# Performance work log

Measured on AMD Instinct MI355X. Metric: run time of the kernel, lower is better.

## Reference

```python
import jax, jax.numpy as jnp
import numpy as np

B = 256   # batch (bs)
N = 6890  # SMPL vertices
J = 24    # joints (root + 23)
NB = 10   # betas
P = 100   # points per foot plane
PARENTS = np.array([-1,0,0,0,1,2,3,4,5,6,7,8,9,9,9,12,13,14,16,17,18,19,20,21], dtype=np.int64)


def setup_inputs() -> dict:
    key = jax.random.key(0)
    ks = jax.random.split(key, 20)
    v_template = jax.random.normal(ks[0], (N, 3), jnp.float32) * 0.3
    shapedirs = jax.random.normal(ks[1], (N, 3, NB), jnp.float32) * 0.01
    Jr = jax.random.uniform(ks[2], (J, N), jnp.float32)
    J_regressor = Jr / Jr.sum(axis=1, keepdims=True)
    lw = jax.random.uniform(ks[3], (N, J), jnp.float32)
    lbs_weights = lw / lw.sum(axis=1, keepdims=True)
    betas = jnp.concatenate([jnp.ones((1, 1), jnp.float32),
                             jax.random.normal(ks[4], (1, NB), jnp.float32) * 0.5], axis=1)
    return dict(
        v_template=v_template, shapedirs=shapedirs, J_regressor=J_regressor,
        lbs_weights=lbs_weights, betas=betas,
        body_pose_wo_foot=jax.random.normal(ks[5], (B, 57), jnp.float32) * 0.2,
        r_back_foot_pose=jax.random.normal(ks[6], (B, 3), jnp.float32) * 0.2,
        r_front_foot_pose=jax.random.normal(ks[7], (B,), jnp.float32) * 0.2,
        l_back_foot_pose=jax.random.normal(ks[8], (B, 3), jnp.float32) * 0.2,
        l_front_foot_pose=jax.random.normal(ks[9], (B,), jnp.float32) * 0.2,
        transl=jax.random.normal(ks[10], (B, 3), jnp.float32) * 0.1,
        global_orient=jax.random.normal(ks[11], (B, 3), jnp.float32) * 0.2,
        init_plane_back_l=jax.random.normal(ks[12], (B, P, 3), jnp.float32) * 0.1,
        init_plane_front_l=jax.random.normal(ks[13], (B, P, 3), jnp.float32) * 0.1,
        init_plane_back_r=jax.random.normal(ks[14], (B, P, 3), jnp.float32) * 0.1,
        init_plane_front_r=jax.random.normal(ks[15], (B, P, 3), jnp.float32) * 0.1,
        parents=jnp.asarray(PARENTS),
        foot_back_l_ids=jax.random.randint(ks[16], (P,), 0, N),
        foot_back_r_ids=jax.random.randint(ks[17], (P,), 0, N),
        foot_front_l_ids=jax.random.randint(ks[18], (P,), 0, N),
        foot_front_r_ids=jax.random.randint(ks[19], (P,), 0, N),
    )


def _rodrigues(rot_vecs):
    # rot_vecs: [M,3] axis-angle -> [M,3,3] rotation matrices (matches SMPL batch_rodrigues)
    angle = jnp.linalg.norm(rot_vecs + 1e-8, axis=1, keepdims=True)  # [M,1]
    rot_dir = rot_vecs / angle
    cos = jnp.cos(angle)[..., None]  # [M,1,1]
    sin = jnp.sin(angle)[..., None]
    rx, ry, rz = rot_dir[:, 0], rot_dir[:, 1], rot_dir[:, 2]
    zeros = jnp.zeros_like(rx)
    K = jnp.stack([zeros, -rz, ry, rz, zeros, -rx, -ry, rx, zeros], axis=1).reshape(-1, 3, 3)
    I = jnp.eye(3, dtype=rot_vecs.dtype)
    return I + sin * K + (1.0 - cos) * jnp.matmul(K, K)


def _forward(v_template, shapedirs, J_regressor, lbs_weights, betas,
             body_pose_wo_foot, r_back_foot_pose, r_front_foot_pose,
             l_back_foot_pose, l_front_foot_pose, transl, global_orient,
             init_plane_back_l, init_plane_front_l, init_plane_back_r, init_plane_front_r,
             ids):
    Bn = body_pose_wo_foot.shape[0]
    dt = v_template.dtype
    # --- update_shape ---
    blend = jnp.einsum('bl,mkl->bmk', betas[:, 1:], shapedirs)            # [1,N,3]
    v_shaped = (v_template[None] + blend) * betas[:, 0][:, None, None]    # [1,N,3]
    J_shaped = jnp.einsum('bik,ji->bjk', v_shaped, J_regressor)           # [1,J,3]
    # --- assemble full pose (foot-joint splicing) ---
    z2 = jnp.zeros((Bn, 2), dt)
    body_pose = jnp.concatenate([
        body_pose_wo_foot[:, :18],              # joints 1..6
        l_back_foot_pose,                       # joint 7
        r_back_foot_pose,                       # joint 8
        body_pose_wo_foot[:, 18:21],            # joint 9
        l_front_foot_pose[:, None], z2,         # joint 10 (x only)
        r_front_foot_pose[:, None], z2,         # joint 11 (x only)
        body_pose_wo_foot[:, 21:]], axis=1)     # joints 12..23
    full_pose = jnp.concatenate([global_orient, body_pose], axis=1)      # [B,72]
    rot = _rodrigues(full_pose.reshape(-1, 3)).reshape(Bn, J, 3, 3)
    # --- batch_rigid_transform ---
    joints = jnp.broadcast_to(J_shaped, (Bn, J, 3))
    rel = jnp.concatenate([joints[:, :1], joints[:, 1:] - joints[:, PARENTS[1:]]], axis=1)
    top = jnp.concatenate([rot, rel[..., None]], axis=-1)                 # [B,J,3,4]
    bottom = jnp.broadcast_to(jnp.array([0., 0., 0., 1.], dt), (Bn, J, 1, 4))
    T_loc = jnp.concatenate([top, bottom], axis=2)                        # [B,J,4,4]
    chain = [T_loc[:, 0]]
    for i in range(1, J):  # fixed 24-joint kinematic chain
        chain.append(chain[int(PARENTS[i])] @ T_loc[:, i])
    transforms = jnp.stack(chain, axis=1)                                 # [B,J,4,4]
    J_transformed = transforms[..., :3, 3]
    init_bone = jnp.einsum('bjmn,bjn->bjm', transforms[..., :3, :3], joints)
    A = transforms.at[..., :3, 3].add(-init_bone)                         # relative transforms
    # --- LBS skinning ---
    T = jnp.einsum('vj,bjmn->bvmn', lbs_weights, A)                       # [B,N,4,4]
    verts = jnp.einsum('bvmn,vn->bvm', T[:, :, :3, :3], v_shaped[0]) + T[:, :, :3, 3] + transl[:, None]
    # --- foot planes ---
    def _plane(idx, init):
        Tp = T[:, idx]                                                    # [B,P,4,4]
        return jnp.einsum('bpmn,bpn->bpm', Tp[:, :, :3, :3], init) + Tp[:, :, :3, 3]
    bl, fl, br, fr = ids
    v_plane = jnp.concatenate([
        _plane(bl, init_plane_back_l), _plane(fl, init_plane_front_l),
        _plane(br, init_plane_back_r), _plane(fr, init_plane_front_r)], axis=1) + transl[:, None]
    return verts, J_transformed, v_plane


def reference(v_template, shapedirs, J_regressor, lbs_weights, betas,
              body_pose_wo_foot, r_back_foot_pose, r_front_foot_pose,
              l_back_foot_pose, l_front_foot_pose, transl, global_orient,
              init_plane_back_l, init_plane_front_l, init_plane_back_r, init_plane_front_r,
              parents, foot_back_l_ids, foot_back_r_ids, foot_front_l_ids, foot_front_r_ids):
    ids = (foot_back_l_ids, foot_front_l_ids, foot_back_r_ids, foot_front_r_ids)
    return _forward(v_template, shapedirs, J_regressor, lbs_weights, betas,
                    body_pose_wo_foot, r_back_foot_pose, r_front_foot_pose,
                    l_back_foot_pose, l_front_foot_pose, transl, global_orient,
                    init_plane_back_l, init_plane_front_l, init_plane_back_r, init_plane_front_r,
                    ids)
```

## Files before the change

kernel.cpp:

```cpp
#include <hip/hip_runtime.h>
#include <stdint.h>

#define NV 6890
#define NJ 24
#define NB_ 256
#define NP 100
#define MP 6912

typedef unsigned short u16;
typedef unsigned int u32;
typedef __attribute__((ext_vector_type(8))) short bf16x8;
typedef __attribute__((ext_vector_type(4))) float f32x4;

__device__ __forceinline__ u16 f2bf(float f) {
    u32 u = __float_as_uint(f);
    u += 0x7FFFu + ((u >> 16) & 1u);
    return (u16)(u >> 16);
}

__constant__ int c_par[24] = {-1,0,0,0,1,2,3,4,5,6,7,8,9,9,9,12,13,14,16,17,18,19,20,21};

#define O_VS 0
#define O_JS 20672
#define O_A  20800
#define O_WT 189056
#define O_AT 852608

#define OUT_JT   5291520
#define OUT_PLN  5309952

__global__ __launch_bounds__(256) void k_shape(const float* __restrict__ vt,
                                               const float* __restrict__ sd,
                                               const float* __restrict__ jreg,
                                               const float* __restrict__ betas,
                                               float* __restrict__ ws) {
    int bx = blockIdx.x;
    float b0 = betas[0];
    if (bx < 81) {
        int idx = bx * 256 + threadIdx.x;
        if (idx < NV * 3) {
            float acc = vt[idx];
            const float* row = sd + (size_t)idx * 10;
#pragma unroll
            for (int l = 0; l < 10; ++l) acc += betas[1 + l] * row[l];
            ws[O_VS + idx] = acc * b0;
        }
        return;
    }
    int j = bx - 81;
    int tid = threadIdx.x;
    float be[10];
#pragma unroll
    for (int l = 0; l < 10; ++l) be[l] = betas[1 + l];
    float s0 = 0.f, s1 = 0.f, s2 = 0.f;
    for (int i = tid; i < NV; i += 256) {
        float w = jreg[(size_t)j * NV + i];
        const float* sr = sd + (size_t)i * 30;
        const float* vr = vt + (size_t)i * 3;
        float c0 = vr[0], c1 = vr[1], c2 = vr[2];
#pragma unroll
        for (int l = 0; l < 10; ++l) {
            c0 += be[l] * sr[l];
            c1 += be[l] * sr[10 + l];
            c2 += be[l] * sr[20 + l];
        }
        s0 += w * (c0 * b0);
        s1 += w * (c1 * b0);
        s2 += w * (c2 * b0);
    }
    __shared__ float r0[256], r1[256], r2[256];
    r0[tid] = s0; r1[tid] = s1; r2[tid] = s2;
    __syncthreads();
    for (int off = 128; off > 0; off >>= 1) {
        if (tid < off) { r0[tid] += r0[tid + off]; r1[tid] += r1[tid + off]; r2[tid] += r2[tid + off]; }
        __syncthreads();
    }
    if (tid == 0) {
        ws[O_JS + j * 3 + 0] = r0[0];
        ws[O_JS + j * 3 + 1] = r1[0];
        ws[O_JS + j * 3 + 2] = r2[0];
    }
}

__global__ __launch_bounds__(256) void k_prep(const float* __restrict__ lw,
                                              const float* __restrict__ bpwf,
                                              const float* __restrict__ rback,
                                              const float* __restrict__ rfront,
                                              const float* __restrict__ lback,
                                              const float* __restrict__ lfront,
                                              const float* __restrict__ gor,
                                              float* __restrict__ ws,
                                              u16* __restrict__ wsu,
                                              float* __restrict__ out) {
    int bx = blockIdx.x;
    if (bx < 2592) {
        int idx = bx * 256 + threadIdx.x;
        int v = idx / 96, k = idx - 96 * v;
        u16 o = 0;
        if (v < NV) {
            int j = k >> 2, n = k & 3;
            float w = lw[(size_t)v * 24 + j];
            float h = (n < 3) ? ws[O_VS + v * 3 + n] : 1.0f;
            o = f2bf(w * h);
        }
        wsu[O_WT + idx] = o;
        return;
    }
    int b = bx - 2592;
    int j = threadIdx.x;
    const float* js = ws + O_JS;
    __shared__ float sT[24][12];
    __shared__ float sJ[24][3];
    if (j < 24) {
        float px, py, pz;
        if (j == 0)      { px = gor[b*3];   py = gor[b*3+1];   pz = gor[b*3+2]; }
        else if (j <= 6) { int o = b*57 + 3*(j-1); px = bpwf[o]; py = bpwf[o+1]; pz = bpwf[o+2]; }
        else if (j == 7) { px = lback[b*3]; py = lback[b*3+1]; pz = lback[b*3+2]; }
        else if (j == 8) { px = rback[b*3]; py = rback[b*3+1]; pz = rback[b*3+2]; }
        else if (j == 9) { int o = b*57 + 18;     px = bpwf[o]; py = bpwf[o+1]; pz = bpwf[o+2]; }
        else if (j == 10){ px = lfront[b];  py = 0.f; pz = 0.f; }
        else if (j == 11){ px = rfront[b];  py = 0.f; pz = 0.f; }
        else             { int o = b*57 + 21 + 3*(j-12); px = bpwf[o]; py = bpwf[o+1]; pz = bpwf[o+2]; }
        float ax = px + 1e-8f, ay = py + 1e-8f, az = pz + 1e-8f;
        float ang = sqrtf(ax*ax + ay*ay + az*az);
        float inv = 1.0f / ang;
        float dx = px * inv, dy = py * inv, dz = pz * inv;
        float c = cosf(ang), s = sinf(ang), t = 1.0f - c;
        sJ[j][0] = js[j*3]; sJ[j][1] = js[j*3+1]; sJ[j][2] = js[j*3+2];
        int p = c_par[j];
        float rx = sJ[j][0], ry = sJ[j][1], rz = sJ[j][2];
        if (p >= 0) { rx -= js[p*3]; ry -= js[p*3+1]; rz -= js[p*3+2]; }
        sT[j][0] = 1.f - t*(dy*dy + dz*dz);
        sT[j][1] = -s*dz + t*dx*dy;
        sT[j][2] =  s*dy + t*dx*dz;
        sT[j][3] = rx;
        sT[j][4] =  s*dz + t*dx*dy;
        sT[j][5] = 1.f - t*(dx*dx + dz*dz);
        sT[j][6] = -s*dx + t*dy*dz;
        sT[j][7] = ry;
        sT[j][8] = -s*dy + t*dx*dz;
        sT[j][9] =  s*dx + t*dy*dz;
        sT[j][10]= 1.f - t*(dx*dx + dy*dy);
        sT[j][11]= rz;
    }
    __syncthreads();
    if (j < 24) {
        int path[12]; int d = 0; int cur = j;
        while (cur >= 0) { path[d++] = cur; cur = c_par[cur]; }
        float g[12];
        int r = path[d - 1];
#pragma unroll
        for (int m = 0; m < 12; ++m) g[m] = sT[r][m];
        for (int i = d - 2; i >= 0; --i) {
            int n = path[i];
            float h[12];
#pragma unroll
            for (int row = 0; row < 3; ++row) {
                float a0 = g[row*4+0], a1 = g[row*4+1], a2 = g[row*4+2], a3 = g[row*4+3];
                h[row*4+0] = a0*sT[n][0] + a1*sT[n][4] + a2*sT[n][8];
                h[row*4+1] = a0*sT[n][1] + a1*sT[n][5] + a2*sT[n][9];
                h[row*4+2] = a0*sT[n][2] + a1*sT[n][6] + a2*sT[n][10];
                h[row*4+3] = a0*sT[n][3] + a1*sT[n][7] + a2*sT[n][11] + a3;
            }
#pragma unroll
            for (int m = 0; m < 12; ++m) g[m] = h[m];
        }
        size_t jo = (size_t)OUT_JT + ((size_t)b * 24 + j) * 3;
        out[jo+0] = g[3]; out[jo+1] = g[7]; out[jo+2] = g[11];
        float jx = sJ[j][0], jy = sJ[j][1], jz = sJ[j][2];
        float Av[12];
        Av[0]=g[0]; Av[1]=g[1]; Av[2]=g[2];   Av[3] = g[3]  - (g[0]*jx + g[1]*jy + g[2]*jz);
        Av[4]=g[4]; Av[5]=g[5]; Av[6]=g[6];   Av[7] = g[7]  - (g[4]*jx + g[5]*jy + g[6]*jz);
        Av[8]=g[8]; Av[9]=g[9]; Av[10]=g[10]; Av[11]= g[11] - (g[8]*jx + g[9]*jy + g[10]*jz);
        float* Ab = ws + O_A + ((size_t)b * 24 + j) * 12;
#pragma unroll
        for (int m = 0; m < 12; ++m) Ab[m] = Av[m];
        u16* at = wsu + O_AT;
#pragma unroll
        for (int m = 0; m < 3; ++m)
#pragma unroll
            for (int n = 0; n < 4; ++n)
                at[(size_t)(b*3 + m) * 96 + j*4 + n] = f2bf(Av[m*4 + n]);
    }
}

__global__ __launch_bounds__(256) void k_main(const u16* __restrict__ wsu,
                                              const float* __restrict__ ws,
                                              const float* __restrict__ lw,
                                              const float* __restrict__ transl,
                                              const int* __restrict__ ids_bl,
                                              const int* __restrict__ ids_fl,
                                              const int* __restrict__ ids_br,
                                              const int* __restrict__ ids_fr,
                                              const float* __restrict__ ip_bl,
                                              const float* __restrict__ ip_fl,
                                              const float* __restrict__ ip_br,
                                              const float* __restrict__ ip_fr,
                                              float* __restrict__ out) {
    if (blockIdx.y < 12) {
        __shared__ float ltile[64][66];
        const u16* wt = wsu + O_WT;
        const u16* at = wsu + O_AT;
        int lane = threadIdx.x & 63;
        int wave = threadIdx.x >> 6;
        int row_in = lane & 15, quad = lane >> 4;
        int v0 = blockIdx.x * 64 + wave * 16;
        int c0 = blockIdx.y * 64;

        f32x4 acc0 = {0.f,0.f,0.f,0.f}, acc1 = acc0, acc2 = acc0, acc3 = acc0;
#pragma unroll
        for (int kc = 0; kc < 96; kc += 32) {
            bf16x8 a  = *(const bf16x8*)(wt + (size_t)(v0 + row_in) * 96 + kc + quad * 8);
            bf16x8 b0 = *(const bf16x8*)(at + (size_t)(c0 +  0 + row_in) * 96 + kc + quad * 8);
            bf16x8 b1 = *(const bf16x8*)(at + (size_t)(c0 + 16 + row_in) * 96 + kc + quad * 8);
            bf16x8 b2 = *(const bf16x8*)(at + (size_t)(c0 + 32 + row_in) * 96 + kc + quad * 8);
            bf16x8 b3 = *(const bf16x8*)(at + (size_t)(c0 + 48 + row_in) * 96 + kc + quad * 8);
            acc0 = __builtin_amdgcn_mfma_f32_16x16x32_bf16(a, b0, acc0, 0, 0, 0);
            acc1 = __builtin_amdgcn_mfma_f32_16x16x32_bf16(a, b1, acc1, 0, 0, 0);
            acc2 = __builtin_amdgcn_mfma_f32_16x16x32_bf16(a, b2, acc2, 0, 0, 0);
            acc3 = __builtin_amdgcn_mfma_f32_16x16x32_bf16(a, b3, acc3, 0, 0, 0);
        }
        int vbase = wave * 16 + quad * 4;
#pragma unroll
        for (int s = 0; s < 4; ++s) {
            f32x4 acc = (s == 0) ? acc0 : (s == 1) ? acc1 : (s == 2) ? acc2 : acc3;
#pragma unroll
            for (int r = 0; r < 4; ++r)
                ltile[vbase + r][s * 16 + row_in] = acc[r];
        }
        __syncthreads();
        int vblk = blockIdx.x * 64;
        int bstart = c0 / 3;
        int bend = (c0 + 63) / 3;
        int tid = threadIdx.x;
        for (int b = bstart; b <= bend; ++b) {
            if (tid < 192) {
                int vl = tid / 3, m = tid - 3 * (tid / 3);
                int cl = b * 3 + m - c0;
                int v = vblk + vl;
                if (cl >= 0 && cl < 64 && v < NV)
                    out[((size_t)b * NV + v) * 3 + m] = ltile[vl][cl] + transl[b * 3 + m];
            }
            if (tid >= 192 && tid < 192 + 64) {
            }
        }
        return;
    }
    for (int idx = blockIdx.x * 256 + threadIdx.x; idx < NB_ * 400; idx += 108 * 256) {
        int b = idx / 400;
        int rr = idx - 400 * b;
        int plane = rr / 100;
        int p = rr - 100 * plane;
        const int* ids   = (plane == 0) ? ids_bl : (plane == 1) ? ids_fl : (plane == 2) ? ids_br : ids_fr;
        const float* ip  = (plane == 0) ? ip_bl  : (plane == 1) ? ip_fl  : (plane == 2) ? ip_br  : ip_fr;
        int vid = ids[p];
        const float* Ab = ws + O_A + (size_t)b * 288;
        const float* w = lw + (size_t)vid * 24;
        float T[12];
#pragma unroll
        for (int m = 0; m < 12; ++m) T[m] = 0.f;
#pragma unroll
        for (int j = 0; j < NJ; ++j) {
            float wj = w[j];
#pragma unroll
            for (int m = 0; m < 12; ++m) T[m] += wj * Ab[j * 12 + m];
        }
        size_t io = ((size_t)b * NP + p) * 3;
        float vx = ip[io+0], vy = ip[io+1], vz = ip[io+2];
        float ox = T[0]*vx + T[1]*vy + T[2]*vz  + T[3]  + transl[b*3+0];
        float oy = T[4]*vx + T[5]*vy + T[6]*vz  + T[7]  + transl[b*3+1];
        float oz = T[8]*vx + T[9]*vy + T[10]*vz + T[11] + transl[b*3+2];
        size_t o = (size_t)OUT_PLN + (size_t)idx * 3;
        out[o+0] = ox; out[o+1] = oy; out[o+2] = oz;
    }
}

extern "C" void kernel_launch(void* const* d_in, const int* in_sizes, int n_in,
                              void* d_out, int out_size, void* d_ws, size_t ws_size,
                              hipStream_t stream) {
    const float* vt     = (const float*)d_in[0];
    const float* sd     = (const float*)d_in[1];
    const float* jreg   = (const float*)d_in[2];
    const float* lw     = (const float*)d_in[3];
    const float* betas  = (const float*)d_in[4];
    const float* bpwf   = (const float*)d_in[5];
    const float* rback  = (const float*)d_in[6];
    const float* rfront = (const float*)d_in[7];
    const float* lback  = (const float*)d_in[8];
    const float* lfront = (const float*)d_in[9];
    const float* transl = (const float*)d_in[10];
    const float* gor    = (const float*)d_in[11];
    const float* ip_bl  = (const float*)d_in[12];
    const float* ip_fl  = (const float*)d_in[13];
    const float* ip_br  = (const float*)d_in[14];
    const float* ip_fr  = (const float*)d_in[15];
    const int* ids_bl = (const int*)d_in[17];
    const int* ids_br = (const int*)d_in[18];
    const int* ids_fl = (const int*)d_in[19];
    const int* ids_fr = (const int*)d_in[20];

    float* ws  = (float*)d_ws;
    u16*   wsu = (u16*)d_ws;
    float* out = (float*)d_out;

    k_shape<<<dim3(81 + 24), 256, 0, stream>>>(vt, sd, jreg, betas, ws);
    k_prep <<<dim3(2592 + 256), 256, 0, stream>>>(lw, bpwf, rback, rfront, lback, lfront, gor,
                                                  ws, wsu, out);
    k_main <<<dim3(108, 13), 256, 0, stream>>>(wsu, ws, lw, transl,
                                               ids_bl, ids_fl, ids_br, ids_fr,
                                               ip_bl, ip_fl, ip_br, ip_fr, out);
}
```

Baseline: 147.8 us.

## Restructure preprocessing stages to shorten the dependency chain

Builds the bf16 weight tile straight from shaped vertices in the first kernel, with one thread per vertex writing 96 values through vector stores. This removes the serial shape → weight-tile dependency and the separate 2592-block pass. The joint regression is split into 8 slices per joint, giving 192 blocks with partial sums that the second kernel reduces. The second kernel also pre-gathers the foot-plane vertex skinning weights so the plane loop reads them contiguously. Each thread now holds a 96-entry u16 buffer, which may spill to scratch.

```diff
diff --git a/kernel.cpp b/kernel.cpp
--- a/kernel.cpp
+++ b/kernel.cpp
@@ -7,6 +7,15 @@
 #define NP 100
 #define MP 6912
 
+#define OUT_JT   5291520
+#define OUT_PLN  5309952
+
+#define O_JP 0
+#define O_A  576
+#define O_PW 74304
+#define O_WT 169984
+#define O_AT 833536
+
 typedef unsigned short u16;
 typedef unsigned int u32;
 typedef __attribute__((ext_vector_type(8))) short bf16x8;
@@ -20,107 +29,127 @@
 
 __constant__ int c_par[24] = {-1,0,0,0,1,2,3,4,5,6,7,8,9,9,9,12,13,14,16,17,18,19,20,21};
 
-#define O_VS 0
-#define O_JS 20672
-#define O_A  20800
-#define O_WT 189056
-#define O_AT 852608
-
-#define OUT_JT   5291520
-#define OUT_PLN  5309952
-
-__global__ __launch_bounds__(256) void k_shape(const float* __restrict__ vt,
-                                               const float* __restrict__ sd,
-                                               const float* __restrict__ jreg,
-                                               const float* __restrict__ betas,
-                                               float* __restrict__ ws) {
-    int bx = blockIdx.x;
-    float b0 = betas[0];
-    if (bx < 81) {
-        int idx = bx * 256 + threadIdx.x;
-        if (idx < NV * 3) {
-            float acc = vt[idx];
-            const float* row = sd + (size_t)idx * 10;
-#pragma unroll
-            for (int l = 0; l < 10; ++l) acc += betas[1 + l] * row[l];
-            ws[O_VS + idx] = acc * b0;
-        }
+struct Params {
+    const float *vt, *sd, *jreg, *lw, *betas, *bpwf, *rback, *rfront,
+                *lback, *lfront, *transl, *gor, *ip_bl, *ip_fl, *ip_br, *ip_fr;
+    const int *ids_bl, *ids_fl, *ids_br, *ids_fr;
+    float* ws;
+    u16* wsu;
+    float* out;
+};
+
+__global__ __launch_bounds__(256) void k_d1(Params P) {
+    int bx = blockIdx.x, tid = threadIdx.x;
+    if (bx < 27) {
+        int v = bx * 256 + tid;
+        u16 buf[96];
+        if (v < NV) {
+            float be[11];
+#pragma unroll
+            for (int l = 0; l < 11; ++l) be[l] = P.betas[l];
+            const float* sr = P.sd + (size_t)v * 30;
+            const float* vr = P.vt + (size_t)v * 3;
+            float vs[3];
+#pragma unroll
+            for (int n = 0; n < 3; ++n) {
+                float acc = vr[n];
+#pragma unroll
+                for (int l = 0; l < 10; ++l) acc += be[1 + l] * sr[n * 10 + l];
+                vs[n] = acc * be[0];
+            }
+            const float* wr = P.lw + (size_t)v * 24;
+#pragma unroll
+            for (int j = 0; j < 24; ++j) {
+                float w = wr[j];
+                buf[j*4+0] = f2bf(w * vs[0]);
+                buf[j*4+1] = f2bf(w * vs[1]);
+                buf[j*4+2] = f2bf(w * vs[2]);
+                buf[j*4+3] = f2bf(w);
+            }
+        } else {
+#pragma unroll
+            for (int m = 0; m < 96; ++m) buf[m] = 0;
+        }
+        uint4* dst = (uint4*)(P.wsu + O_WT + (size_t)v * 96);
+        const uint4* src = (const uint4*)buf;
+#pragma unroll
+        for (int m = 0; m < 12; ++m) dst[m] = src[m];
         return;
     }
-    int j = bx - 81;
-    int tid = threadIdx.x;
-    float be[10];
-#pragma unroll
-    for (int l = 0; l < 10; ++l) be[l] = betas[1 + l];
-    float s0 = 0.f, s1 = 0.f, s2 = 0.f;
-    for (int i = tid; i < NV; i += 256) {
-        float w = jreg[(size_t)j * NV + i];
-        const float* sr = sd + (size_t)i * 30;
-        const float* vr = vt + (size_t)i * 3;
-        float c0 = vr[0], c1 = vr[1], c2 = vr[2];
-#pragma unroll
-        for (int l = 0; l < 10; ++l) {
-            c0 += be[l] * sr[l];
-            c1 += be[l] * sr[10 + l];
-            c2 += be[l] * sr[20 + l];
-        }
-        s0 += w * (c0 * b0);
-        s1 += w * (c1 * b0);
-        s2 += w * (c2 * b0);
-    }
-    __shared__ float r0[256], r1[256], r2[256];
-    r0[tid] = s0; r1[tid] = s1; r2[tid] = s2;
-    __syncthreads();
-    for (int off = 128; off > 0; off >>= 1) {
-        if (tid < off) { r0[tid] += r0[tid + off]; r1[tid] += r1[tid + off]; r2[tid] += r2[tid + off]; }
+    {
+        int idx = bx - 27;
+        int j = idx >> 3, sl = idx & 7;
+        int i0 = sl * 862, i1 = (i0 + 862 < NV) ? i0 + 862 : NV;
+        float b0 = P.betas[0];
+        float be[10];
+#pragma unroll
+        for (int l = 0; l < 10; ++l) be[l] = P.betas[1 + l];
+        float s0 = 0.f, s1 = 0.f, s2 = 0.f;
+        for (int i = i0 + tid; i < i1; i += 256) {
+            float w = P.jreg[(size_t)j * NV + i];
+            const float* sr = P.sd + (size_t)i * 30;
+            const float* vr = P.vt + (size_t)i * 3;
+            float c0 = vr[0], c1 = vr[1], c2 = vr[2];
+#pragma unroll
+            for (int l = 0; l < 10; ++l) {
+                c0 += be[l] * sr[l];
+                c1 += be[l] * sr[10 + l];
+                c2 += be[l] * sr[20 + l];
+            }
+            s0 += w * (c0 * b0); s1 += w * (c1 * b0); s2 += w * (c2 * b0);
+        }
+        __shared__ float r0[256], r1[256], r2[256];
+        r0[tid] = s0; r1[tid] = s1; r2[tid] = s2;
         __syncthreads();
-    }
-    if (tid == 0) {
-        ws[O_JS + j * 3 + 0] = r0[0];
-        ws[O_JS + j * 3 + 1] = r1[0];
-        ws[O_JS + j * 3 + 2] = r2[0];
-    }
-}
-
-__global__ __launch_bounds__(256) void k_prep(const float* __restrict__ lw,
-                                              const float* __restrict__ bpwf,
-                                              const float* __restrict__ rback,
-                                              const float* __restrict__ rfront,
-                                              const float* __restrict__ lback,
-                                              const float* __restrict__ lfront,
-                                              const float* __restrict__ gor,
-                                              float* __restrict__ ws,
-                                              u16* __restrict__ wsu,
-                                              float* __restrict__ out) {
-    int bx = blockIdx.x;
-    if (bx < 2592) {
-        int idx = bx * 256 + threadIdx.x;
-        int v = idx / 96, k = idx - 96 * v;
-        u16 o = 0;
-        if (v < NV) {
-            int j = k >> 2, n = k & 3;
-            float w = lw[(size_t)v * 24 + j];
-            float h = (n < 3) ? ws[O_VS + v * 3 + n] : 1.0f;
-            o = f2bf(w * h);
-        }
-        wsu[O_WT + idx] = o;
+        for (int off = 128; off > 0; off >>= 1) {
+            if (tid < off) { r0[tid] += r0[tid+off]; r1[tid] += r1[tid+off]; r2[tid] += r2[tid+off]; }
+            __syncthreads();
+        }
+        if (tid == 0) {
+            P.ws[O_JP + (j*8 + sl)*3 + 0] = r0[0];
+            P.ws[O_JP + (j*8 + sl)*3 + 1] = r1[0];
+            P.ws[O_JP + (j*8 + sl)*3 + 2] = r2[0];
+        }
+    }
+}
+
+__global__ __launch_bounds__(256) void k_d2(Params P) {
+    int bx = blockIdx.x, tid = threadIdx.x;
+    if (bx >= NB_) {
+        int q = (bx - NB_) * 256 + tid;
+        if (q < 9600) {
+            int rr = q / 24, j = q - 24 * rr;
+            int plane = rr / 100, p = rr - 100 * plane;
+            const int* ids = (plane == 0) ? P.ids_bl : (plane == 1) ? P.ids_fl
+                           : (plane == 2) ? P.ids_br : P.ids_fr;
+            P.ws[O_PW + q] = P.lw[(size_t)ids[p] * 24 + j];
+        }
         return;
     }
-    int b = bx - 2592;
-    int j = threadIdx.x;
-    const float* js = ws + O_JS;
+    int b = bx;
+    __shared__ float js[72];
     __shared__ float sT[24][12];
     __shared__ float sJ[24][3];
+    if (tid < 72) {
+        int j = tid / 3, cc = tid - 3 * j;
+        float a = 0.f;
+#pragma unroll
+        for (int s = 0; s < 8; ++s) a += P.ws[O_JP + (j*8 + s)*3 + cc];
+        js[tid] = a;
+    }
+    __syncthreads();
+    int j = tid;
     if (j < 24) {
         float px, py, pz;
-        if (j == 0)      { px = gor[b*3];   py = gor[b*3+1];   pz = gor[b*3+2]; }
-        else if (j <= 6) { int o = b*57 + 3*(j-1); px = bpwf[o]; py = bpwf[o+1]; pz = bpwf[o+2]; }
-        else if (j == 7) { px = lback[b*3]; py = lback[b*3+1]; pz = lback[b*3+2]; }
-        else if (j == 8) { px = rback[b*3]; py = rback[b*3+1]; pz = rback[b*3+2]; }
-        else if (j == 9) { int o = b*57 + 18;     px = bpwf[o]; py = bpwf[o+1]; pz = bpwf[o+2]; }
-        else if (j == 10){ px = lfront[b];  py = 0.f; pz = 0.f; }
-        else if (j == 11){ px = rfront[b];  py = 0.f; pz = 0.f; }
-        else             { int o = b*57 + 21 + 3*(j-12); px = bpwf[o]; py = bpwf[o+1]; pz = bpwf[o+2]; }
+        const float* bp = P.bpwf;
+        if (j == 0)      { px = P.gor[b*3];   py = P.gor[b*3+1];   pz = P.gor[b*3+2]; }
+        else if (j <= 6) { int o = b*57 + 3*(j-1); px = bp[o]; py = bp[o+1]; pz = bp[o+2]; }
+        else if (j == 7) { px = P.lback[b*3]; py = P.lback[b*3+1]; pz = P.lback[b*3+2]; }
+        else if (j == 8) { px = P.rback[b*3]; py = P.rback[b*3+1]; pz = P.rback[b*3+2]; }
+        else if (j == 9) { int o = b*57 + 18;     px = bp[o]; py = bp[o+1]; pz = bp[o+2]; }
+        else if (j == 10){ px = P.lfront[b];  py = 0.f; pz = 0.f; }
+        else if (j == 11){ px = P.rfront[b];  py = 0.f; pz = 0.f; }
+        else             { int o = b*57 + 21 + 3*(j-12); px = bp[o]; py = bp[o+1]; pz = bp[o+2]; }
         float ax = px + 1e-8f, ay = py + 1e-8f, az = pz + 1e-8f;
         float ang = sqrtf(ax*ax + ay*ay + az*az);
         float inv = 1.0f / ang;
@@ -166,16 +195,16 @@
             for (int m = 0; m < 12; ++m) g[m] = h[m];
         }
         size_t jo = (size_t)OUT_JT + ((size_t)b * 24 + j) * 3;
-        out[jo+0] = g[3]; out[jo+1] = g[7]; out[jo+2] = g[11];
+        P.out[jo+0] = g[3]; P.out[jo+1] = g[7]; P.out[jo+2] = g[11];
         float jx = sJ[j][0], jy = sJ[j][1], jz = sJ[j][2];
         float Av[12];
         Av[0]=g[0]; Av[1]=g[1]; Av[2]=g[2];   Av[3] = g[3]  - (g[0]*jx + g[1]*jy + g[2]*jz);
         Av[4]=g[4]; Av[5]=g[5]; Av[6]=g[6];   Av[7] = g[7]  - (g[4]*jx + g[5]*jy + g[6]*jz);
         Av[8]=g[8]; Av[9]=g[9]; Av[10]=g[10]; Av[11]= g[11] - (g[8]*jx + g[9]*jy + g[10]*jz);
-        float* Ab = ws + O_A + ((size_t)b * 24 + j) * 12;
+        float* Ab = P.ws + O_A + ((size_t)b * 24 + j) * 12;
 #pragma unroll
         for (int m = 0; m < 12; ++m) Ab[m] = Av[m];
-        u16* at = wsu + O_AT;
+        u16* at = P.wsu + O_AT;
 #pragma unroll
         for (int m = 0; m < 3; ++m)
 #pragma unroll
@@ -184,25 +213,14 @@
     }
 }
 
-__global__ __launch_bounds__(256) void k_main(const u16* __restrict__ wsu,
-                                              const float* __restrict__ ws,
-                                              const float* __restrict__ lw,
-                                              const float* __restrict__ transl,
-                                              const int* __restrict__ ids_bl,
-                                              const int* __restrict__ ids_fl,
-                                              const int* __restrict__ ids_br,
-                                              const int* __restrict__ ids_fr,
-                                              const float* __restrict__ ip_bl,
-                                              const float* __restrict__ ip_fl,
-                                              const float* __restrict__ ip_br,
-                                              const float* __restrict__ ip_fr,
-                                              float* __restrict__ out) {
+__global__ __launch_bounds__(256) void k_d3(Params P) {
     if (blockIdx.y < 12) {
         __shared__ float ltile[64][66];
-        const u16* wt = wsu + O_WT;
-        const u16* at = wsu + O_AT;
-        int lane = threadIdx.x & 63;
-        int wave = threadIdx.x >> 6;
+        const u16* wt = P.wsu + O_WT;
+        const u16* at = P.wsu + O_AT;
+        int tid = threadIdx.x;
+        int lane = tid & 63;
+        int wave = tid >> 6;
         int row_in = lane & 15, quad = lane >> 4;
         int v0 = blockIdx.x * 64 + wave * 16;
         int c0 = blockIdx.y * 64;
@@ -232,16 +250,13 @@
         int vblk = blockIdx.x * 64;
         int bstart = c0 / 3;
         int bend = (c0 + 63) / 3;
-        int tid = threadIdx.x;
         for (int b = bstart; b <= bend; ++b) {
             if (tid < 192) {
                 int vl = tid / 3, m = tid - 3 * (tid / 3);
                 int cl = b * 3 + m - c0;
                 int v = vblk + vl;
                 if (cl >= 0 && cl < 64 && v < NV)
-                    out[((size_t)b * NV + v) * 3 + m] = ltile[vl][cl] + transl[b * 3 + m];
-            }
-            if (tid >= 192 && tid < 192 + 64) {
+                    P.out[((size_t)b * NV + v) * 3 + m] = ltile[vl][cl] + P.transl[b * 3 + m];
             }
         }
         return;
@@ -249,13 +264,8 @@
     for (int idx = blockIdx.x * 256 + threadIdx.x; idx < NB_ * 400; idx += 108 * 256) {
         int b = idx / 400;
         int rr = idx - 400 * b;
-        int plane = rr / 100;
-        int p = rr - 100 * plane;
-        const int* ids   = (plane == 0) ? ids_bl : (plane == 1) ? ids_fl : (plane == 2) ? ids_br : ids_fr;
-        const float* ip  = (plane == 0) ? ip_bl  : (plane == 1) ? ip_fl  : (plane == 2) ? ip_br  : ip_fr;
-        int vid = ids[p];
-        const float* Ab = ws + O_A + (size_t)b * 288;
-        const float* w = lw + (size_t)vid * 24;
+        const float* w  = P.ws + O_PW + rr * 24;
+        const float* Ab = P.ws + O_A + (size_t)b * 288;
         float T[12];
 #pragma unroll
         for (int m = 0; m < 12; ++m) T[m] = 0.f;
@@ -265,48 +275,48 @@
 #pragma unroll
             for (int m = 0; m < 12; ++m) T[m] += wj * Ab[j * 12 + m];
         }
+        int plane = rr / 100, p = rr - 100 * plane;
+        const float* ip = (plane == 0) ? P.ip_bl : (plane == 1) ? P.ip_fl
+                        : (plane == 2) ? P.ip_br : P.ip_fr;
         size_t io = ((size_t)b * NP + p) * 3;
         float vx = ip[io+0], vy = ip[io+1], vz = ip[io+2];
-        float ox = T[0]*vx + T[1]*vy + T[2]*vz  + T[3]  + transl[b*3+0];
-        float oy = T[4]*vx + T[5]*vy + T[6]*vz  + T[7]  + transl[b*3+1];
-        float oz = T[8]*vx + T[9]*vy + T[10]*vz + T[11] + transl[b*3+2];
+        float ox = T[0]*vx + T[1]*vy + T[2]*vz  + T[3]  + P.transl[b*3+0];
+        float oy = T[4]*vx + T[5]*vy + T[6]*vz  + T[7]  + P.transl[b*3+1];
+        float oz = T[8]*vx + T[9]*vy + T[10]*vz + T[11] + P.transl[b*3+2];
         size_t o = (size_t)OUT_PLN + (size_t)idx * 3;
-        out[o+0] = ox; out[o+1] = oy; out[o+2] = oz;
+        P.out[o+0] = ox; P.out[o+1] = oy; P.out[o+2] = oz;
     }
 }
 
 extern "C" void kernel_launch(void* const* d_in, const int* in_sizes, int n_in,
                               void* d_out, int out_size, void* d_ws, size_t ws_size,
                               hipStream_t stream) {
-    const float* vt     = (const float*)d_in[0];
-    const float* sd     = (const float*)d_in[1];
-    const float* jreg   = (const float*)d_in[2];
-    const float* lw     = (const float*)d_in[3];
-    const float* betas  = (const float*)d_in[4];
-    const float* bpwf   = (const float*)d_in[5];
-    const float* rback  = (const float*)d_in[6];
-    const float* rfront = (const float*)d_in[7];
-    const float* lback  = (const float*)d_in[8];
-    const float* lfront = (const float*)d_in[9];
-    const float* transl = (const float*)d_in[10];
-    const float* gor    = (const float*)d_in[11];
-    const float* ip_bl  = (const float*)d_in[12];
-    const float* ip_fl  = (const float*)d_in[13];
-    const float* ip_br  = (const float*)d_in[14];
-    const float* ip_fr  = (const float*)d_in[15];
-    const int* ids_bl = (const int*)d_in[17];
-    const int* ids_br = (const int*)d_in[18];
-    const int* ids_fl = (const int*)d_in[19];
-    const int* ids_fr = (const int*)d_in[20];
-
-    float* ws  = (float*)d_ws;
-    u16*   wsu = (u16*)d_ws;
-    float* out = (float*)d_out;
-
-    k_shape<<<dim3(81 + 24), 256, 0, stream>>>(vt, sd, jreg, betas, ws);
-    k_prep <<<dim3(2592 + 256), 256, 0, stream>>>(lw, bpwf, rback, rfront, lback, lfront, gor,
-                                                  ws, wsu, out);
-    k_main <<<dim3(108, 13), 256, 0, stream>>>(wsu, ws, lw, transl,
-                                               ids_bl, ids_fl, ids_br, ids_fr,
-                                               ip_bl, ip_fl, ip_br, ip_fr, out);
-}
+    Params P;
+    P.vt     = (const float*)d_in[0];
+    P.sd     = (const float*)d_in[1];
+    P.jreg   = (const float*)d_in[2];
+    P.lw     = (const float*)d_in[3];
+    P.betas  = (const float*)d_in[4];
+    P.bpwf   = (const float*)d_in[5];
+    P.rback  = (const float*)d_in[6];
+    P.rfront = (const float*)d_in[7];
+    P.lback  = (const float*)d_in[8];
+    P.lfront = (const float*)d_in[9];
+    P.transl = (const float*)d_in[10];
+    P.gor    = (const float*)d_in[11];
+    P.ip_bl  = (const float*)d_in[12];
+    P.ip_fl  = (const float*)d_in[13];
+    P.ip_br  = (const float*)d_in[14];
+    P.ip_fr  = (const float*)d_in[15];
+    P.ids_bl = (const int*)d_in[17];
+    P.ids_br = (const int*)d_in[18];
+    P.ids_fl = (const int*)d_in[19];
+    P.ids_fr = (const int*)d_in[20];
+    P.ws  = (float*)d_ws;
+    P.wsu = (u16*)d_ws;
+    P.out = (float*)d_out;
+
+    k_d1<<<dim3(27 + 192), 256, 0, stream>>>(P);
+    k_d2<<<dim3(NB_ + 38), 256, 0, stream>>>(P);
+    k_d3<<<dim3(108, 13), 256, 0, stream>>>(P);
+}
```

Result: no change. 145.9 us, median of 2 (-1.3%).
